# Performance work log

Hardware: AMD Instinct MI355X
Metric: run time of the kernel (lower is better)

## Reference

```python
import jax, jax.numpy as jnp
import numpy as np

NUM_GRAPHS = 512  # number of distinct graph ids in batch


def _gcn_agg(x, batch):
    # mm(block_full_adj, x) == per-graph sum broadcast back to nodes
    sums = jax.ops.segment_sum(x, batch, num_segments=NUM_GRAPHS)
    return sums[batch]


def setup_inputs() -> dict:
    key = jax.random.key(0)
    ks = jax.random.split(key, 8)
    N, D = 100000, 128
    H = 2 * D
    x = jax.random.normal(ks[0], (N, D), dtype=jnp.float32)
    batch = jnp.sort(jax.random.randint(ks[1], (N,), 0, NUM_GRAPHS)).astype(jnp.int64)
    s = 0.05
    W1 = jax.random.normal(ks[2], (D, H), dtype=jnp.float32) * s
    b1 = jax.random.normal(ks[3], (H,), dtype=jnp.float32) * s
    W2 = jax.random.normal(ks[4], (H, H), dtype=jnp.float32) * s
    b2 = jax.random.normal(ks[5], (H,), dtype=jnp.float32) * s
    Wc = jax.random.normal(ks[6], (H, 1), dtype=jnp.float32) * s
    bc = jax.random.normal(ks[7], (1,), dtype=jnp.float32) * s
    return {"x": x, "batch": batch, "W1": W1, "b1": b1, "W2": W2, "b2": b2, "Wc": Wc, "bc": bc}


def reference(x, batch, W1, b1, W2, b2, Wc, bc):
    h = jax.nn.relu(_gcn_agg(x, batch) @ W1 + b1)          # GCN layer 1
    h = jax.nn.relu(_gcn_agg(h, batch) @ W2 + b2)          # GCN layer 2
    c = h @ Wc + bc                                         # confidence head
    sp = jax.nn.softplus(c)
    return sp / (1.0 + sp)
```

## Files before the change

### kernel.cpp

```cpp
#include <hip/hip_runtime.h>
#include <math.h>

#define NUM_GRAPHS 512
#define D 128
#define HDIM 256
#define K 4
#define GPB 4

#define DETECT_IS64(batch32, N, tid, sWave, sIs64)                         \
    {                                                                      \
        int cap = (N) < 1024 ? (N) : 1024;                                 \
        int local = 0x7fffffff;                                            \
        for (int i = (tid); i < cap; i += 256)                             \
            if ((batch32)[i] != 0) { local = i; break; }                   \
        for (int off = 32; off > 0; off >>= 1)                             \
            local = min(local, __shfl_down(local, off, 64));               \
        if (((tid) & 63) == 0) (sWave)[(tid) >> 6] = local;                \
        __syncthreads();                                                   \
        if ((tid) == 0) {                                                  \
            int j = min(min((sWave)[0], (sWave)[1]),                       \
                        min((sWave)[2], (sWave)[3]));                      \
            (sIs64) = (j != 0x7fffffff && j + 1 < (N) &&                   \
                       (batch32)[j + 1] == 0) ? 1 : 0;                     \
        }                                                                  \
        __syncthreads();                                                   \
    }

__device__ __forceinline__ int lower_bound_g(const int* batch32, int is64,
                                             int N, int target)
{
    const long long* batch64 = (const long long*)batch32;
    int lo = 0, hi = N;
    while (lo < hi) {
        int m = (lo + hi) >> 1;
        long long v = is64 ? batch64[m] : (long long)batch32[m];
        if (v < (long long)target) lo = m + 1; else hi = m;
    }
    return lo;
}

__global__ __launch_bounds__(256) void seg_sum(
    const float* __restrict__ x, const int* __restrict__ batch32,
    float4* __restrict__ partial4, int N)
{
    const int blk = blockIdx.x;
    const int g   = blk / K;
    const int k   = blk % K;
    const int tid = threadIdx.x;

    __shared__ int    sIs64;
    __shared__ int    sWave[4];
    __shared__ int    sStart, sEnd;
    __shared__ float4 part[256];

    DETECT_IS64(batch32, N, tid, sWave, sIs64);
    const int is64 = sIs64;

    if (tid < 2) {
        int lo = lower_bound_g(batch32, is64, N, g + tid);
        if (tid == 0) sStart = lo; else sEnd = lo;
    }
    __syncthreads();

    const int start = sStart, end = sEnd;
    const int n   = end - start;
    const int per = (n + K - 1) / K;
    const int r0  = start + k * per;
    const int r1  = min(r0 + per, end);

    const int r  = tid >> 5;
    const int c4 = tid & 31;
    float4 acc = make_float4(0.f, 0.f, 0.f, 0.f);
    const float4* x4 = (const float4*)x;
    for (int row = r0 + r; row < r1; row += 8) {
        float4 v = x4[row * 32 + c4];
        acc.x += v.x; acc.y += v.y; acc.z += v.z; acc.w += v.w;
    }
    part[tid] = acc;
    __syncthreads();
    for (int s = 4; s >= 1; s >>= 1) {
        if (r < s) {
            float4 o = part[tid + s * 32];
            float4 m = part[tid];
            m.x += o.x; m.y += o.y; m.z += o.z; m.w += o.w;
            part[tid] = m;
        }
        __syncthreads();
    }
    if (tid < 32)
        partial4[blk * 32 + tid] = part[tid];
}

__global__ __launch_bounds__(256) void mlp_scatter(
    const float* __restrict__ partial, const int* __restrict__ batch32,
    const float* __restrict__ W1, const float* __restrict__ b1,
    const float* __restrict__ W2, const float* __restrict__ b2,
    const float* __restrict__ Wc, const float* __restrict__ bc,
    float* __restrict__ out, int N)
{
    const int g0  = blockIdx.x * GPB;
    const int tid = threadIdx.x;

    __shared__ int   sIs64;
    __shared__ int   sWave[4];
    __shared__ int   sBound[GPB + 1];
    __shared__ float sS[GPB][D];
    __shared__ float sH[GPB][HDIM];
    __shared__ float sRed[4][GPB];
    __shared__ float sCval[GPB];

    DETECT_IS64(batch32, N, tid, sWave, sIs64);
    const int is64 = sIs64;

    if (tid <= GPB)
        sBound[tid] = lower_bound_g(batch32, is64, N, g0 + tid);
    __syncthreads();

    if (tid < D) {
        #pragma unroll
        for (int j = 0; j < GPB; ++j) {
            float s = 0.f;
            #pragma unroll
            for (int k = 0; k < K; ++k)
                s += partial[((g0 + j) * K + k) * D + tid];
            sS[j][tid] = s;
        }
    }
    __syncthreads();

    float a1[GPB];
    {
        float bb = b1[tid];
        #pragma unroll
        for (int j = 0; j < GPB; ++j) a1[j] = bb;
    }
    for (int k = 0; k < D; ++k) {
        float w = W1[k * HDIM + tid];
        #pragma unroll
        for (int j = 0; j < GPB; ++j) a1[j] = fmaf(sS[j][k], w, a1[j]);
    }
    #pragma unroll
    for (int j = 0; j < GPB; ++j) {
        float cnt = (float)(sBound[j + 1] - sBound[j]);
        sH[j][tid] = fmaxf(a1[j], 0.f) * cnt;
    }
    __syncthreads();

    float a2[GPB];
    {
        float bb = b2[tid];
        #pragma unroll
        for (int j = 0; j < GPB; ++j) a2[j] = bb;
    }
    for (int k = 0; k < HDIM; ++k) {
        float w = W2[k * HDIM + tid];
        #pragma unroll
        for (int j = 0; j < GPB; ++j) a2[j] = fmaf(sH[j][k], w, a2[j]);
    }
    float wc = Wc[tid];
    float v[GPB];
    #pragma unroll
    for (int j = 0; j < GPB; ++j) v[j] = fmaxf(a2[j], 0.f) * wc;
    for (int off = 32; off > 0; off >>= 1) {
        #pragma unroll
        for (int j = 0; j < GPB; ++j) v[j] += __shfl_down(v[j], off, 64);
    }
    if ((tid & 63) == 0) {
        #pragma unroll
        for (int j = 0; j < GPB; ++j) sRed[tid >> 6][j] = v[j];
    }
    __syncthreads();
    if (tid < GPB) {
        float cc = sRed[0][tid] + sRed[1][tid] + sRed[2][tid] + sRed[3][tid]
                 + bc[0];
        float m  = fmaxf(cc, 0.f);
        float sp = m + log1pf(expf(-fabsf(cc)));
        sCval[tid] = sp / (1.f + sp);
    }
    __syncthreads();

    #pragma unroll
    for (int j = 0; j < GPB; ++j) {
        float val = sCval[j];
        for (int i = sBound[j] + tid; i < sBound[j + 1]; i += 256)
            out[i] = val;
    }
}

extern "C" void kernel_launch(void* const* d_in, const int* in_sizes, int n_in,
                              void* d_out, int out_size, void* d_ws, size_t ws_size,
                              hipStream_t stream)
{
    const float* x   = (const float*)d_in[0];
    const int*   bat = (const int*)d_in[1];
    const float* W1  = (const float*)d_in[2];
    const float* b1  = (const float*)d_in[3];
    const float* W2  = (const float*)d_in[4];
    const float* b2  = (const float*)d_in[5];
    const float* Wc  = (const float*)d_in[6];
    const float* bc  = (const float*)d_in[7];
    float* out = (float*)d_out;
    const int N = in_sizes[0] / D;

    float* partial = (float*)d_ws;

    seg_sum<<<NUM_GRAPHS * K, 256, 0, stream>>>(x, bat, (float4*)partial, N);
    mlp_scatter<<<NUM_GRAPHS / GPB, 256, 0, stream>>>(partial, bat,
                                                      W1, b1, W2, b2, Wc, bc,
                                                      out, N);
}
```

Measured before the change: 126.1 us.

## Retune split factors, simplify int64 detection, unroll loads and loops

Doubles the number of seg_sum blocks per graph (K 4->8) and halves graphs per MLP block (GPB 4->2) to spread work over more CUs. Replaces the block-wide int64 detection scan and its two barriers with a single-element check of the last batch entry. It also makes the row accumulation 2-way unrolled with two accumulators, uses all 256 threads to gather partial sums, unrolls the GEMV loops, and merges the output scatter into one loop. The new int64 check assumes the high word of the last entry is zero and the low word nonzero, which holds for sorted non-negative ids but not for every possible input.

```diff
diff --git a/kernel.cpp b/kernel.cpp
--- a/kernel.cpp
+++ b/kernel.cpp
@@ -4,30 +4,17 @@
 #define NUM_GRAPHS 512
 #define D 128
 #define HDIM 256
-#define K 4
-#define GPB 4
-
-#define DETECT_IS64(batch32, N, tid, sWave, sIs64)                         \
-    {                                                                      \
-        int cap = (N) < 1024 ? (N) : 1024;                                 \
-        int local = 0x7fffffff;                                            \
-        for (int i = (tid); i < cap; i += 256)                             \
-            if ((batch32)[i] != 0) { local = i; break; }                   \
-        for (int off = 32; off > 0; off >>= 1)                             \
-            local = min(local, __shfl_down(local, off, 64));               \
-        if (((tid) & 63) == 0) (sWave)[(tid) >> 6] = local;                \
-        __syncthreads();                                                   \
-        if ((tid) == 0) {                                                  \
-            int j = min(min((sWave)[0], (sWave)[1]),                       \
-                        min((sWave)[2], (sWave)[3]));                      \
-            (sIs64) = (j != 0x7fffffff && j + 1 < (N) &&                   \
-                       (batch32)[j + 1] == 0) ? 1 : 0;                     \
-        }                                                                  \
-        __syncthreads();                                                   \
-    }
-
-__device__ __forceinline__ int lower_bound_g(const int* batch32, int is64,
-                                             int N, int target)
+#define K 8
+#define GPB 2
+
+__device__ __forceinline__ int detect_is64(const int* __restrict__ b, int N)
+{
+    const int j = ((N - 1) & 1) ? (N - 1) : (N - 2);
+    return b[j] == 0;
+}
+
+__device__ __forceinline__ int lower_bound_g(const int* __restrict__ batch32,
+                                             int is64, int N, int target)
 {
     const long long* batch64 = (const long long*)batch32;
     int lo = 0, hi = N;
@@ -44,19 +31,15 @@
     float4* __restrict__ partial4, int N)
 {
     const int blk = blockIdx.x;
-    const int g   = blk / K;
-    const int k   = blk % K;
+    const int g   = blk >> 3;
+    const int k   = blk & 7;
     const int tid = threadIdx.x;
 
-    __shared__ int    sIs64;
-    __shared__ int    sWave[4];
     __shared__ int    sStart, sEnd;
     __shared__ float4 part[256];
 
-    DETECT_IS64(batch32, N, tid, sWave, sIs64);
-    const int is64 = sIs64;
-
     if (tid < 2) {
+        const int is64 = detect_is64(batch32, N);
         int lo = lower_bound_g(batch32, is64, N, g + tid);
         if (tid == 0) sStart = lo; else sEnd = lo;
     }
@@ -70,13 +53,23 @@
 
     const int r  = tid >> 5;
     const int c4 = tid & 31;
-    float4 acc = make_float4(0.f, 0.f, 0.f, 0.f);
+    float4 a0 = make_float4(0.f, 0.f, 0.f, 0.f);
+    float4 a1 = make_float4(0.f, 0.f, 0.f, 0.f);
     const float4* x4 = (const float4*)x;
-    for (int row = r0 + r; row < r1; row += 8) {
-        float4 v = x4[row * 32 + c4];
-        acc.x += v.x; acc.y += v.y; acc.z += v.z; acc.w += v.w;
-    }
-    part[tid] = acc;
+    int row = r0 + r;
+    for (; row + 8 < r1; row += 16) {
+        float4 v0 = x4[row * 32 + c4];
+        float4 v1 = x4[(row + 8) * 32 + c4];
+        a0.x += v0.x; a0.y += v0.y; a0.z += v0.z; a0.w += v0.w;
+        a1.x += v1.x; a1.y += v1.y; a1.z += v1.z; a1.w += v1.w;
+    }
+    if (row < r1) {
+        float4 v0 = x4[row * 32 + c4];
+        a0.x += v0.x; a0.y += v0.y; a0.z += v0.z; a0.w += v0.w;
+    }
+    a0.x += a1.x; a0.y += a1.y; a0.z += a1.z; a0.w += a1.w;
+
+    part[tid] = a0;
     __syncthreads();
     for (int s = 4; s >= 1; s >>= 1) {
         if (r < s) {
@@ -101,30 +94,25 @@
     const int g0  = blockIdx.x * GPB;
     const int tid = threadIdx.x;
 
-    __shared__ int   sIs64;
-    __shared__ int   sWave[4];
     __shared__ int   sBound[GPB + 1];
     __shared__ float sS[GPB][D];
     __shared__ float sH[GPB][HDIM];
     __shared__ float sRed[4][GPB];
     __shared__ float sCval[GPB];
 
-    DETECT_IS64(batch32, N, tid, sWave, sIs64);
-    const int is64 = sIs64;
-
-    if (tid <= GPB)
+    if (tid <= GPB) {
+        const int is64 = detect_is64(batch32, N);
         sBound[tid] = lower_bound_g(batch32, is64, N, g0 + tid);
-    __syncthreads();
-
-    if (tid < D) {
-        #pragma unroll
-        for (int j = 0; j < GPB; ++j) {
-            float s = 0.f;
-            #pragma unroll
-            for (int k = 0; k < K; ++k)
-                s += partial[((g0 + j) * K + k) * D + tid];
-            sS[j][tid] = s;
-        }
+    }
+
+    {
+        const int j = tid >> 7;
+        const int dcol = tid & (D - 1);
+        float s = 0.f;
+        #pragma unroll
+        for (int k = 0; k < K; ++k)
+            s += partial[((g0 + j) * K + k) * D + dcol];
+        sS[j][dcol] = s;
     }
     __syncthreads();
 
@@ -134,6 +122,7 @@
         #pragma unroll
         for (int j = 0; j < GPB; ++j) a1[j] = bb;
     }
+    #pragma unroll 16
     for (int k = 0; k < D; ++k) {
         float w = W1[k * HDIM + tid];
         #pragma unroll
@@ -152,6 +141,7 @@
         #pragma unroll
         for (int j = 0; j < GPB; ++j) a2[j] = bb;
     }
+    #pragma unroll 16
     for (int k = 0; k < HDIM; ++k) {
         float w = W2[k * HDIM + tid];
         #pragma unroll
@@ -179,11 +169,11 @@
     }
     __syncthreads();
 
-    #pragma unroll
-    for (int j = 0; j < GPB; ++j) {
-        float val = sCval[j];
-        for (int i = sBound[j] + tid; i < sBound[j + 1]; i += 256)
-            out[i] = val;
+    {
+        const int s0 = sBound[0], s1 = sBound[1], s2 = sBound[GPB];
+        const float v0 = sCval[0], v1 = sCval[1];
+        for (int i = s0 + tid; i < s2; i += 256)
+            out[i] = (i < s1) ? v0 : v1;
     }
 }
 
```

After: 119.0 us. 5.7% less time.
